# Optimization experiments

Hardware: AMD Instinct MI355X
Metric: run time of the kernel (lower is better)

The kernel has to match this reference:

```python
import jax, jax.numpy as jnp
import numpy as np

BN_EPS = 1e-5
INTERP_EPS = 1e-8


def _bn_relu(x, g, b, m, v):
    # eval-mode BatchNorm1d over channel dim (last axis here) + ReLU
    return jax.nn.relu((x - m) * (g / jnp.sqrt(v + BN_EPS)) + b)


def setup_inputs() -> dict:
    key = jax.random.key(0)
    ks = jax.random.split(key, 12)
    B, N, S, C1, C2 = 4, 16384, 1024, 128, 256
    Cin = C1 + C2  # 384
    H1, H2 = 256, 128
    inp = {
        "xyz1": jax.random.normal(ks[0], (B, N, 3), jnp.float32),
        "xyz2": jax.random.normal(ks[1], (B, S, 3), jnp.float32),
        "points1": jax.random.normal(ks[2], (B, N, C1), jnp.float32),
        "points2": jax.random.normal(ks[3], (B, S, C2), jnp.float32),
        # Conv1d(k=1, bias=False) weights: (out_ch, in_ch)
        "w1": jax.random.normal(ks[4], (H1, Cin), jnp.float32) * (1.0 / np.sqrt(Cin)),
        "g1": jax.random.uniform(ks[5], (H1,), jnp.float32, 0.5, 1.5),
        "b1": jax.random.normal(ks[6], (H1,), jnp.float32) * 0.1,
        "m1": jax.random.normal(ks[7], (H1,), jnp.float32) * 0.1,
        "v1": jax.random.uniform(ks[8], (H1,), jnp.float32, 0.5, 1.5),
        "w2": jax.random.normal(ks[9], (H2, H1), jnp.float32) * (1.0 / np.sqrt(H1)),
        "g2": jax.random.uniform(ks[10], (H2,), jnp.float32, 0.5, 1.5),
        "b2": jax.random.normal(ks[11], (H2,), jnp.float32) * 0.1,
        "m2": jnp.zeros((H2,), jnp.float32),
        "v2": jnp.ones((H2,), jnp.float32),
    }
    return inp


def reference(xyz1, xyz2, points1, points2, w1, g1, b1, m1, v1, w2, g2, b2, m2, v2):
    B, N, _ = xyz1.shape
    S = xyz2.shape[1]
    # squared pairwise distances (B, N, S) via ||a||^2 + ||b||^2 - 2 a.b
    sq = (
        jnp.sum(xyz1 * xyz1, -1)[:, :, None]
        + jnp.sum(xyz2 * xyz2, -1)[:, None, :]
        - 2.0 * jnp.einsum("bnd,bsd->bns", xyz1, xyz2)
    )
    neg_d, idx = jax.lax.top_k(-sq, 3)  # 3 nearest neighbors
    dists = -neg_d  # (B, N, 3) squared distances, ascending
    recip = 1.0 / (dists + INTERP_EPS)
    weight = recip / jnp.sum(recip, -1, keepdims=True)  # (B, N, 3)
    # gather neighbor features: (B, N, 3, C2)
    gathered = points2[jnp.arange(B)[:, None, None], idx]
    interpolated = jnp.einsum("bnk,bnkc->bnc", weight, gathered)
    new_points = jnp.concatenate([points1, interpolated], axis=-1)  # (B, N, Cin)
    h = _bn_relu(jnp.einsum("bnc,dc->bnd", new_points, w1), g1, b1, m1, v1)
    out = _bn_relu(jnp.einsum("bnc,dc->bnd", h, w2), g2, b2, m2, v2)
    return out
```

## Files before the change

### kernel.cpp

```cpp
#include <hip/hip_runtime.h>
#include <math.h>

#define B_    4
#define N_    16384
#define S_    1024
#define C1_   128
#define C2_   256
#define CIN_  384
#define H1_   256
#define H2_   128
#define BN_EPS_     1e-5f
#define INTERP_EPS_ 1e-8f

typedef _Float16 f16;
typedef _Float16 f16x4 __attribute__((ext_vector_type(4)));
typedef _Float16 f16x8 __attribute__((ext_vector_type(8)));
typedef float    f32x4 __attribute__((ext_vector_type(4)));
typedef unsigned int u32;

#define GLD16(g, l) \
  __builtin_amdgcn_global_load_lds((const __attribute__((address_space(1))) void*)(g), \
                                   (__attribute__((address_space(3))) void*)(l), 16, 0, 0)

#define WS_IDXP 0
#define WS_W    262144
#define WS_XI   1048576
#define WS_H    34603008
#define WS_W1F  68157440
#define WS_W2F  68354048
#define WS_SC1  68419584
#define WS_SH1  68420608
#define WS_SC2  68421632
#define WS_SH2  68422144

__global__ __launch_bounds__(256) void prep_kernel(
    const float* __restrict__ w1, const float* __restrict__ w2,
    const float* __restrict__ g1, const float* __restrict__ b1,
    const float* __restrict__ m1, const float* __restrict__ v1,
    const float* __restrict__ g2, const float* __restrict__ b2,
    const float* __restrict__ m2, const float* __restrict__ v2,
    f16* __restrict__ w1f, f16* __restrict__ w2f,
    float* __restrict__ sc1, float* __restrict__ sh1,
    float* __restrict__ sc2, float* __restrict__ sh2)
{
    const int t = blockIdx.x * 256 + threadIdx.x;
    if (t < 98304) {
        w1f[t] = (f16)w1[t];
    } else if (t < 131072) {
        w2f[t - 98304] = (f16)w2[t - 98304];
    } else if (t < 131328) {
        const int c = t - 131072;
        const float s = g1[c] / sqrtf(v1[c] + BN_EPS_);
        sc1[c] = s; sh1[c] = b1[c] - m1[c] * s;
    } else if (t < 131456) {
        const int c = t - 131328;
        const float s = g2[c] / sqrtf(v2[c] + BN_EPS_);
        sc2[c] = s; sh2[c] = b2[c] - m2[c] * s;
    }
}

__device__ __forceinline__ u32 umin_(u32 a, u32 b) { return a < b ? a : b; }
__device__ __forceinline__ u32 umax_(u32 a, u32 b) { return a > b ? a : b; }

#define KINS(k) do { \
    u32 c1 = umax_(s0, (k)); s0 = umin_(s0, (k)); \
    u32 c2 = umax_(s1, c1);  s1 = umin_(s1, c1);  \
    u32 c3 = umax_(s2, c2);  s2 = umin_(s2, c2);  \
    u32 c4 = umax_(s3, c3);  s3 = umin_(s3, c3);  \
    s4 = umin_(s4, c4); } while (0)

#define CSWAP(a_, b_) do { \
    if (rd[b_] < rd[a_] || (rd[b_] == rd[a_] && ri[b_] < ri[a_])) { \
      double td = rd[a_]; rd[a_] = rd[b_]; rd[b_] = td; \
      int ti = ri[a_]; ri[a_] = ri[b_]; ri[b_] = ti; } } while (0)

__global__ __launch_bounds__(256) void topk_kernel(
    const float* __restrict__ xyz1, const float* __restrict__ xyz2,
    u32* __restrict__ idxp_out, float* __restrict__ w_out)
{
    __shared__ float4 q[S_ + 8];
    const int b     = blockIdx.x >> 9;
    const int pbase = (blockIdx.x & 511) << 5;
    const int t     = threadIdx.x;

    for (int i = t; i < S_; i += 256) {
        const float* s = &xyz2[((size_t)b * S_ + i) * 3];
        float4 v; v.x = s[0]; v.y = s[1]; v.z = s[2]; v.w = 0.0f;
        q[i + (i >> 7)] = v;
    }
    __syncthreads();

    const int p     = pbase + (t >> 3);
    const int chunk = t & 7;
    const int qb    = chunk * 129;
    const int ebase = chunk << 7;
    const float* pp = &xyz1[((size_t)b * N_ + p) * 3];
    const float px = pp[0], py = pp[1], pz = pp[2];

    u32 s0 = 0xFFFFFFFFu, s1 = 0xFFFFFFFFu, s2 = 0xFFFFFFFFu,
        s3 = 0xFFFFFFFFu, s4 = 0xFFFFFFFFu;

    for (int i = 0; i < 128; i += 4) {
        #pragma unroll
        for (int u = 0; u < 4; ++u) {
            const float4 c = q[qb + i + u];
            const float dx = px - c.x, dy = py - c.y, dz = pz - c.z;
            const float dd = fmaf(dx, dx, fmaf(dy, dy, dz * dz));
            const u32 k = (__float_as_uint(dd) & 0xFFFFFC00u) | (u32)(ebase + i + u);
            KINS(k);
        }
    }

    #pragma unroll
    for (int msk = 1; msk <= 4; msk <<= 1) {
        u32 e0 = __shfl_xor(s0, msk), e1 = __shfl_xor(s1, msk);
        u32 e2 = __shfl_xor(s2, msk), e3 = __shfl_xor(s3, msk);
        u32 e4 = __shfl_xor(s4, msk);
        KINS(e0); KINS(e1); KINS(e2); KINS(e3); KINS(e4);
    }

    if (chunk == 0) {
        const double px6 = px, py6 = py, pz6 = pz;
        double rd[5]; int ri[5];
        const u32 ks[5] = {s0, s1, s2, s3, s4};
        #pragma unroll
        for (int j = 0; j < 5; ++j) {
            const int si = (int)(ks[j] & 1023u); ri[j] = si;
            const float4 c = q[si + (si >> 7)];
            const double dx = px6 - (double)c.x, dy = py6 - (double)c.y, dz = pz6 - (double)c.z;
            rd[j] = dx * dx + dy * dy + dz * dz;
        }
        CSWAP(0,1); CSWAP(1,2); CSWAP(0,1); CSWAP(2,3); CSWAP(1,2);
        CSWAP(0,1); CSWAP(3,4); CSWAP(2,3); CSWAP(1,2); CSWAP(0,1);
        const float r0 = 1.0f / ((float)rd[0] + INTERP_EPS_);
        const float r1 = 1.0f / ((float)rd[1] + INTERP_EPS_);
        const float r2 = 1.0f / ((float)rd[2] + INTERP_EPS_);
        const float rs = r0 + r1 + r2;
        const int row = b * N_ + p;
        idxp_out[row] = (u32)ri[0] | ((u32)ri[1] << 10) | ((u32)ri[2] << 20);
        w_out[row * 3 + 0] = r0 / rs;
        w_out[row * 3 + 1] = r1 / rs;
        w_out[row * 3 + 2] = r2 / rs;
    }
}

__global__ __launch_bounds__(256) void interp_kernel(
    const float* __restrict__ points2, const u32* __restrict__ idxp,
    const float* __restrict__ wts, f16* __restrict__ xi)
{
    const int row  = blockIdx.x * 8 + (threadIdx.x >> 5);
    const int lane = threadIdx.x & 31;
    const int bb   = row >> 14;
    const u32 u    = idxp[row];
    const int i0 = (int)(u & 1023u), i1 = (int)((u >> 10) & 1023u), i2 = (int)(u >> 20);
    const float w0 = wts[row * 3], w1w = wts[row * 3 + 1], w2w = wts[row * 3 + 2];
    const float* p2b = points2 + (size_t)bb * S_ * C2_;
    const int c0 = lane * 8;

    const float4 a0 = *(const float4*)&p2b[i0 * C2_ + c0];
    const float4 a1 = *(const float4*)&p2b[i0 * C2_ + c0 + 4];
    const float4 b0 = *(const float4*)&p2b[i1 * C2_ + c0];
    const float4 b1 = *(const float4*)&p2b[i1 * C2_ + c0 + 4];
    const float4 d0 = *(const float4*)&p2b[i2 * C2_ + c0];
    const float4 d1 = *(const float4*)&p2b[i2 * C2_ + c0 + 4];

    f16x8 o;
    o[0] = (f16)fmaf(w0, a0.x, fmaf(w1w, b0.x, w2w * d0.x));
    o[1] = (f16)fmaf(w0, a0.y, fmaf(w1w, b0.y, w2w * d0.y));
    o[2] = (f16)fmaf(w0, a0.z, fmaf(w1w, b0.z, w2w * d0.z));
    o[3] = (f16)fmaf(w0, a0.w, fmaf(w1w, b0.w, w2w * d0.w));
    o[4] = (f16)fmaf(w0, a1.x, fmaf(w1w, b1.x, w2w * d1.x));
    o[5] = (f16)fmaf(w0, a1.y, fmaf(w1w, b1.y, w2w * d1.y));
    o[6] = (f16)fmaf(w0, a1.z, fmaf(w1w, b1.z, w2w * d1.z));
    o[7] = (f16)fmaf(w0, a1.w, fmaf(w1w, b1.w, w2w * d1.w));
    *(f16x8*)&xi[(size_t)row * C2_ + c0] = o;
}

__device__ __forceinline__ void mfma_step1(const f16* As, const f16* Bs,
                                           f32x4 (&acc)[4][8],
                                           int wr, int wc, int lrow, int lhi)
{
    f16x8 af[4], bf[8];
    #pragma unroll
    for (int m = 0; m < 4; ++m)
        af[m] = *(const f16x8*)&As[(wr * 64 + m * 16 + lrow) * 32 + lhi * 8];
    #pragma unroll
    for (int n = 0; n < 8; ++n)
        bf[n] = *(const f16x8*)&Bs[(wc * 128 + n * 16 + lrow) * 32 + lhi * 8];
    #pragma unroll
    for (int m = 0; m < 4; ++m)
        #pragma unroll
        for (int n = 0; n < 8; ++n)
            acc[m][n] = __builtin_amdgcn_mfma_f32_16x16x32_f16(af[m], bf[n], acc[m][n], 0, 0, 0);
}

__global__ __launch_bounds__(256, 2) void gemm1_kernel(
    const float* __restrict__ points1, const f16* __restrict__ xi,
    const f16* __restrict__ w1f,
    const float* __restrict__ sc1v, const float* __restrict__ sh1v,
    f16* __restrict__ h)
{
    __shared__ __align__(16) f16 As[2 * 128 * 32];
    __shared__ __align__(16) f16 Bs[2 * 256 * 32];

    const int t = threadIdx.x;
    const int w = t >> 6;
    const int lane = t & 63;
    const int wr = w >> 1, wc = w & 1;
    const int lrow = lane & 15, lhi = lane >> 4;
    const int rowbase = blockIdx.x * 128;

    const int srow = t >> 1, khalf = t & 1;
    const float* p1r = points1 + (size_t)(rowbase + srow) * C1_;

    f32x4 acc[4][8] = {};
    float4 pre0, pre1, pre2, pre3;

    {
        const float* src = p1r + khalf * 16;
        pre0 = *(const float4*)(src + 0);
        pre1 = *(const float4*)(src + 4);
        pre2 = *(const float4*)(src + 8);
        pre3 = *(const float4*)(src + 12);
        f16* asrow = As + srow * 32 + khalf * 16;
        f16x4 o0 = {(f16)pre0.x, (f16)pre0.y, (f16)pre0.z, (f16)pre0.w};
        f16x4 o1 = {(f16)pre1.x, (f16)pre1.y, (f16)pre1.z, (f16)pre1.w};
        f16x4 o2 = {(f16)pre2.x, (f16)pre2.y, (f16)pre2.z, (f16)pre2.w};
        f16x4 o3 = {(f16)pre3.x, (f16)pre3.y, (f16)pre3.z, (f16)pre3.w};
        *(f16x4*)(asrow + 0) = o0; *(f16x4*)(asrow + 4) = o1;
        *(f16x4*)(asrow + 8) = o2; *(f16x4*)(asrow + 12) = o3;
        #pragma unroll
        for (int j = 0; j < 4; ++j) {
            const int c = j * 256 + t;
            GLD16(w1f + (size_t)(c >> 2) * CIN_ + (c & 3) * 8,
                  (char*)Bs + (j * 4096 + w * 1024));
        }
    }
    __syncthreads();

    for (int step = 0; step < 12; ++step) {
        const int pb = step & 1, nb = pb ^ 1;
        const int nkb = (step + 1) * 32;
        const bool has_next = (step < 11);
        const bool nextA = (nkb < C1_);

        if (has_next) {
            if (nextA) {
                const float* src = p1r + nkb + khalf * 16;
                pre0 = *(const float4*)(src + 0);
                pre1 = *(const float4*)(src + 4);
                pre2 = *(const float4*)(src + 8);
                pre3 = *(const float4*)(src + 12);
            } else {
                const int kk = nkb - C1_;
                #pragma unroll
                for (int j = 0; j < 2; ++j) {
                    const int c = j * 256 + t;
                    GLD16(xi + (size_t)(rowbase + (c >> 2)) * C2_ + kk + (c & 3) * 8,
                          (char*)As + (nb * 8192 + j * 4096 + w * 1024));
                }
            }
            #pragma unroll
            for (int j = 0; j < 4; ++j) {
                const int c = j * 256 + t;
                GLD16(w1f + (size_t)(c >> 2) * CIN_ + nkb + (c & 3) * 8,
                      (char*)Bs + (nb * 16384 + j * 4096 + w * 1024));
            }
        }

        mfma_step1(As + pb * 4096, Bs + pb * 8192, acc, wr, wc, lrow, lhi);

        if (has_next && nextA) {
            f16* asrow = As + nb * 4096 + srow * 32 + khalf * 16;
            f16x4 o0 = {(f16)pre0.x, (f16)pre0.y, (f16)pre0.z, (f16)pre0.w};
            f16x4 o1 = {(f16)pre1.x, (f16)pre1.y, (f16)pre1.z, (f16)pre1.w};
            f16x4 o2 = {(f16)pre2.x, (f16)pre2.y, (f16)pre2.z, (f16)pre2.w};
            f16x4 o3 = {(f16)pre3.x, (f16)pre3.y, (f16)pre3.z, (f16)pre3.w};
            *(f16x4*)(asrow + 0) = o0; *(f16x4*)(asrow + 4) = o1;
            *(f16x4*)(asrow + 8) = o2; *(f16x4*)(asrow + 12) = o3;
        }
        __syncthreads();
    }

    #pragma unroll
    for (int n = 0; n < 8; ++n) {
        const int col = wc * 128 + n * 16 + lrow;
        const float sc = sc1v[col], sh = sh1v[col];
        #pragma unroll
        for (int m = 0; m < 4; ++m) {
            const int row0 = rowbase + wr * 64 + m * 16 + lhi * 4;
            #pragma unroll
            for (int i = 0; i < 4; ++i) {
                const float v = fmaxf(fmaf(acc[m][n][i], sc, sh), 0.0f);
                h[(size_t)(row0 + i) * H1_ + col] = (f16)v;
            }
        }
    }
}

__global__ __launch_bounds__(256, 2) void gemm2_kernel(
    const f16* __restrict__ hin, const f16* __restrict__ w2f,
    const float* __restrict__ sc2v, const float* __restrict__ sh2v,
    float* __restrict__ out)
{
    __shared__ __align__(16) f16 As[2 * 128 * 32];
    __shared__ __align__(16) f16 Bs[2 * 128 * 32];

    const int t = threadIdx.x;
    const int w = t >> 6;
    const int lane = t & 63;
    const int wr = w >> 1, wc = w & 1;
    const int lrow = lane & 15, lhi = lane >> 4;
    const int rowbase = blockIdx.x * 128;

    f32x4 acc[4][4] = {};

    #pragma unroll
    for (int j = 0; j < 2; ++j) {
        const int c = j * 256 + t;
        GLD16(hin + (size_t)(rowbase + (c >> 2)) * H1_ + (c & 3) * 8,
              (char*)As + (j * 4096 + w * 1024));
        GLD16(w2f + (size_t)(c >> 2) * H1_ + (c & 3) * 8,
              (char*)Bs + (j * 4096 + w * 1024));
    }
    __syncthreads();

    for (int step = 0; step < 8; ++step) {
        const int pb = step & 1, nb = pb ^ 1;
        const int nkb = (step + 1) * 32;

        if (step < 7) {
            #pragma unroll
            for (int j = 0; j < 2; ++j) {
                const int c = j * 256 + t;
                GLD16(hin + (size_t)(rowbase + (c >> 2)) * H1_ + nkb + (c & 3) * 8,
                      (char*)As + (nb * 8192 + j * 4096 + w * 1024));
                GLD16(w2f + (size_t)(c >> 2) * H1_ + nkb + (c & 3) * 8,
                      (char*)Bs + (nb * 8192 + j * 4096 + w * 1024));
            }
        }

        const f16* Ac = As + pb * 4096;
        const f16* Bc = Bs + pb * 4096;
        f16x8 af[4], bf[4];
        #pragma unroll
        for (int m = 0; m < 4; ++m)
            af[m] = *(const f16x8*)&Ac[(wr * 64 + m * 16 + lrow) * 32 + lhi * 8];
        #pragma unroll
        for (int n = 0; n < 4; ++n)
            bf[n] = *(const f16x8*)&Bc[(wc * 64 + n * 16 + lrow) * 32 + lhi * 8];
        #pragma unroll
        for (int m = 0; m < 4; ++m)
            #pragma unroll
            for (int n = 0; n < 4; ++n)
                acc[m][n] = __builtin_amdgcn_mfma_f32_16x16x32_f16(af[m], bf[n], acc[m][n], 0, 0, 0);

        __syncthreads();
    }

    #pragma unroll
    for (int n = 0; n < 4; ++n) {
        const int col = wc * 64 + n * 16 + lrow;
        const float sc = sc2v[col], sh = sh2v[col];
        #pragma unroll
        for (int m = 0; m < 4; ++m) {
            const int row0 = rowbase + wr * 64 + m * 16 + lhi * 4;
            #pragma unroll
            for (int i = 0; i < 4; ++i) {
                out[(size_t)(row0 + i) * H2_ + col] = fmaxf(fmaf(acc[m][n][i], sc, sh), 0.0f);
            }
        }
    }
}

extern "C" void kernel_launch(void* const* d_in, const int* in_sizes, int n_in,
                              void* d_out, int out_size, void* d_ws, size_t ws_size,
                              hipStream_t stream) {
    const float* xyz1    = (const float*)d_in[0];
    const float* xyz2    = (const float*)d_in[1];
    const float* points1 = (const float*)d_in[2];
    const float* points2 = (const float*)d_in[3];
    const float* w1      = (const float*)d_in[4];
    const float* g1      = (const float*)d_in[5];
    const float* b1      = (const float*)d_in[6];
    const float* m1      = (const float*)d_in[7];
    const float* v1      = (const float*)d_in[8];
    const float* w2      = (const float*)d_in[9];
    const float* g2      = (const float*)d_in[10];
    const float* b2      = (const float*)d_in[11];
    const float* m2      = (const float*)d_in[12];
    const float* v2      = (const float*)d_in[13];
    float* out = (float*)d_out;

    char* ws = (char*)d_ws;
    u32*   idxp_ws = (u32*)(ws + WS_IDXP);
    float* w_ws    = (float*)(ws + WS_W);
    f16*   xi_ws   = (f16*)(ws + WS_XI);
    f16*   h_ws    = (f16*)(ws + WS_H);
    f16*   w1f     = (f16*)(ws + WS_W1F);
    f16*   w2f     = (f16*)(ws + WS_W2F);
    float* sc1     = (float*)(ws + WS_SC1);
    float* sh1     = (float*)(ws + WS_SH1);
    float* sc2     = (float*)(ws + WS_SC2);
    float* sh2     = (float*)(ws + WS_SH2);

    topk_kernel<<<dim3(B_ * (N_ / 32)), dim3(256), 0, stream>>>(xyz1, xyz2, idxp_ws, w_ws);
    prep_kernel<<<dim3(514), dim3(256), 0, stream>>>(w1, w2, g1, b1, m1, v1,
                                                     g2, b2, m2, v2,
                                                     w1f, w2f, sc1, sh1, sc2, sh2);
    interp_kernel<<<dim3(B_ * N_ / 8), dim3(256), 0, stream>>>(points2, idxp_ws, w_ws, xi_ws);
    gemm1_kernel<<<dim3(512), dim3(256), 0, stream>>>(points1, xi_ws, w1f, sc1, sh1, h_ws);
    gemm2_kernel<<<dim3(512), dim3(256), 0, stream>>>(h_ws, w2f, sc2, sh2, out);
}
```

Baseline: 187.6 us.

## Fuse topk+interp+prep into one kernel and gemm1+gemm2 via LDS-resident hidden

Merges the kNN top-k search, weight/BN preparation and feature interpolation into a single front kernel, handing neighbor indices and weights through shared memory instead of global workspace. Fuses the two MLP GEMMs so the hidden activation tile stays in swizzled LDS rather than going through a global f16 buffer. This removes two kernel launches, the idx/weight round trip and the large hidden-activation write and read. In exchange the MLP kernel needs 80KB of dynamic shared memory, which may reduce occupancy. It also relies on the front kernel's prep blocks finishing before mlp_kernel starts, which stream order guarantees.

Result: faster. 183.9 us (-2.0%).

```diff
diff --git a/kernel.cpp b/kernel.cpp
--- a/kernel.cpp
+++ b/kernel.cpp
@@ -22,10 +22,7 @@
   __builtin_amdgcn_global_load_lds((const __attribute__((address_space(1))) void*)(g), \
                                    (__attribute__((address_space(3))) void*)(l), 16, 0, 0)
 
-#define WS_IDXP 0
-#define WS_W    262144
 #define WS_XI   1048576
-#define WS_H    34603008
 #define WS_W1F  68157440
 #define WS_W2F  68354048
 #define WS_SC1  68419584
@@ -33,32 +30,6 @@
 #define WS_SC2  68421632
 #define WS_SH2  68422144
 
-__global__ __launch_bounds__(256) void prep_kernel(
-    const float* __restrict__ w1, const float* __restrict__ w2,
-    const float* __restrict__ g1, const float* __restrict__ b1,
-    const float* __restrict__ m1, const float* __restrict__ v1,
-    const float* __restrict__ g2, const float* __restrict__ b2,
-    const float* __restrict__ m2, const float* __restrict__ v2,
-    f16* __restrict__ w1f, f16* __restrict__ w2f,
-    float* __restrict__ sc1, float* __restrict__ sh1,
-    float* __restrict__ sc2, float* __restrict__ sh2)
-{
-    const int t = blockIdx.x * 256 + threadIdx.x;
-    if (t < 98304) {
-        w1f[t] = (f16)w1[t];
-    } else if (t < 131072) {
-        w2f[t - 98304] = (f16)w2[t - 98304];
-    } else if (t < 131328) {
-        const int c = t - 131072;
-        const float s = g1[c] / sqrtf(v1[c] + BN_EPS_);
-        sc1[c] = s; sh1[c] = b1[c] - m1[c] * s;
-    } else if (t < 131456) {
-        const int c = t - 131328;
-        const float s = g2[c] / sqrtf(v2[c] + BN_EPS_);
-        sc2[c] = s; sh2[c] = b2[c] - m2[c] * s;
-    }
-}
-
 __device__ __forceinline__ u32 umin_(u32 a, u32 b) { return a < b ? a : b; }
 __device__ __forceinline__ u32 umax_(u32 a, u32 b) { return a > b ? a : b; }
 
@@ -74,14 +45,45 @@
       double td = rd[a_]; rd[a_] = rd[b_]; rd[b_] = td; \
       int ti = ri[a_]; ri[a_] = ri[b_]; ri[b_] = ti; } } while (0)
 
-__global__ __launch_bounds__(256) void topk_kernel(
+__global__ __launch_bounds__(256) void front_kernel(
     const float* __restrict__ xyz1, const float* __restrict__ xyz2,
-    u32* __restrict__ idxp_out, float* __restrict__ w_out)
+    const float* __restrict__ points2,
+    const float* __restrict__ w1, const float* __restrict__ w2,
+    const float* __restrict__ g1, const float* __restrict__ b1,
+    const float* __restrict__ m1, const float* __restrict__ v1,
+    const float* __restrict__ g2, const float* __restrict__ b2,
+    const float* __restrict__ m2, const float* __restrict__ v2,
+    f16* __restrict__ xi, f16* __restrict__ w1f, f16* __restrict__ w2f,
+    float* __restrict__ sc1, float* __restrict__ sh1,
+    float* __restrict__ sc2, float* __restrict__ sh2)
 {
+    const int bid = blockIdx.x;
+    const int t   = threadIdx.x;
+
+    if (bid >= 2048) {
+        const int tg = (bid - 2048) * 256 + t;
+        if (tg < 98304) {
+            w1f[tg] = (f16)w1[tg];
+        } else if (tg < 131072) {
+            w2f[tg - 98304] = (f16)w2[tg - 98304];
+        } else if (tg < 131328) {
+            const int c = tg - 131072;
+            const float s = g1[c] / sqrtf(v1[c] + BN_EPS_);
+            sc1[c] = s; sh1[c] = b1[c] - m1[c] * s;
+        } else if (tg < 131456) {
+            const int c = tg - 131328;
+            const float s = g2[c] / sqrtf(v2[c] + BN_EPS_);
+            sc2[c] = s; sh2[c] = b2[c] - m2[c] * s;
+        }
+        return;
+    }
+
     __shared__ float4 q[S_ + 8];
-    const int b     = blockIdx.x >> 9;
-    const int pbase = (blockIdx.x & 511) << 5;
-    const int t     = threadIdx.x;
+    __shared__ int   idr[32][3];
+    __shared__ float wtr[32][3];
+
+    const int b     = bid >> 9;
+    const int pbase = (bid & 511) << 5;
 
     for (int i = t; i < S_; i += 256) {
         const float* s = &xyz2[((size_t)b * S_ + i) * 3];
@@ -90,90 +92,91 @@
     }
     __syncthreads();
 
-    const int p     = pbase + (t >> 3);
-    const int chunk = t & 7;
-    const int qb    = chunk * 129;
-    const int ebase = chunk << 7;
-    const float* pp = &xyz1[((size_t)b * N_ + p) * 3];
-    const float px = pp[0], py = pp[1], pz = pp[2];
-
-    u32 s0 = 0xFFFFFFFFu, s1 = 0xFFFFFFFFu, s2 = 0xFFFFFFFFu,
-        s3 = 0xFFFFFFFFu, s4 = 0xFFFFFFFFu;
-
-    for (int i = 0; i < 128; i += 4) {
-        #pragma unroll
-        for (int u = 0; u < 4; ++u) {
-            const float4 c = q[qb + i + u];
-            const float dx = px - c.x, dy = py - c.y, dz = pz - c.z;
-            const float dd = fmaf(dx, dx, fmaf(dy, dy, dz * dz));
-            const u32 k = (__float_as_uint(dd) & 0xFFFFFC00u) | (u32)(ebase + i + u);
-            KINS(k);
-        }
-    }
-
-    #pragma unroll
-    for (int msk = 1; msk <= 4; msk <<= 1) {
-        u32 e0 = __shfl_xor(s0, msk), e1 = __shfl_xor(s1, msk);
-        u32 e2 = __shfl_xor(s2, msk), e3 = __shfl_xor(s3, msk);
-        u32 e4 = __shfl_xor(s4, msk);
-        KINS(e0); KINS(e1); KINS(e2); KINS(e3); KINS(e4);
-    }
-
-    if (chunk == 0) {
-        const double px6 = px, py6 = py, pz6 = pz;
-        double rd[5]; int ri[5];
-        const u32 ks[5] = {s0, s1, s2, s3, s4};
-        #pragma unroll
-        for (int j = 0; j < 5; ++j) {
-            const int si = (int)(ks[j] & 1023u); ri[j] = si;
-            const float4 c = q[si + (si >> 7)];
-            const double dx = px6 - (double)c.x, dy = py6 - (double)c.y, dz = pz6 - (double)c.z;
-            rd[j] = dx * dx + dy * dy + dz * dz;
-        }
-        CSWAP(0,1); CSWAP(1,2); CSWAP(0,1); CSWAP(2,3); CSWAP(1,2);
-        CSWAP(0,1); CSWAP(3,4); CSWAP(2,3); CSWAP(1,2); CSWAP(0,1);
-        const float r0 = 1.0f / ((float)rd[0] + INTERP_EPS_);
-        const float r1 = 1.0f / ((float)rd[1] + INTERP_EPS_);
-        const float r2 = 1.0f / ((float)rd[2] + INTERP_EPS_);
-        const float rs = r0 + r1 + r2;
-        const int row = b * N_ + p;
-        idxp_out[row] = (u32)ri[0] | ((u32)ri[1] << 10) | ((u32)ri[2] << 20);
-        w_out[row * 3 + 0] = r0 / rs;
-        w_out[row * 3 + 1] = r1 / rs;
-        w_out[row * 3 + 2] = r2 / rs;
-    }
-}
-
-__global__ __launch_bounds__(256) void interp_kernel(
-    const float* __restrict__ points2, const u32* __restrict__ idxp,
-    const float* __restrict__ wts, f16* __restrict__ xi)
-{
-    const int row  = blockIdx.x * 8 + (threadIdx.x >> 5);
-    const int lane = threadIdx.x & 31;
-    const int bb   = row >> 14;
-    const u32 u    = idxp[row];
-    const int i0 = (int)(u & 1023u), i1 = (int)((u >> 10) & 1023u), i2 = (int)(u >> 20);
-    const float w0 = wts[row * 3], w1w = wts[row * 3 + 1], w2w = wts[row * 3 + 2];
-    const float* p2b = points2 + (size_t)bb * S_ * C2_;
-    const int c0 = lane * 8;
-
-    const float4 a0 = *(const float4*)&p2b[i0 * C2_ + c0];
-    const float4 a1 = *(const float4*)&p2b[i0 * C2_ + c0 + 4];
-    const float4 b0 = *(const float4*)&p2b[i1 * C2_ + c0];
-    const float4 b1 = *(const float4*)&p2b[i1 * C2_ + c0 + 4];
-    const float4 d0 = *(const float4*)&p2b[i2 * C2_ + c0];
-    const float4 d1 = *(const float4*)&p2b[i2 * C2_ + c0 + 4];
-
-    f16x8 o;
-    o[0] = (f16)fmaf(w0, a0.x, fmaf(w1w, b0.x, w2w * d0.x));
-    o[1] = (f16)fmaf(w0, a0.y, fmaf(w1w, b0.y, w2w * d0.y));
-    o[2] = (f16)fmaf(w0, a0.z, fmaf(w1w, b0.z, w2w * d0.z));
-    o[3] = (f16)fmaf(w0, a0.w, fmaf(w1w, b0.w, w2w * d0.w));
-    o[4] = (f16)fmaf(w0, a1.x, fmaf(w1w, b1.x, w2w * d1.x));
-    o[5] = (f16)fmaf(w0, a1.y, fmaf(w1w, b1.y, w2w * d1.y));
-    o[6] = (f16)fmaf(w0, a1.z, fmaf(w1w, b1.z, w2w * d1.z));
-    o[7] = (f16)fmaf(w0, a1.w, fmaf(w1w, b1.w, w2w * d1.w));
-    *(f16x8*)&xi[(size_t)row * C2_ + c0] = o;
+    {
+        const int p     = pbase + (t >> 3);
+        const int chunk = t & 7;
+        const int qb    = chunk * 129;
+        const int ebase = chunk << 7;
+        const float* pp = &xyz1[((size_t)b * N_ + p) * 3];
+        const float px = pp[0], py = pp[1], pz = pp[2];
+
+        u32 s0 = 0xFFFFFFFFu, s1 = 0xFFFFFFFFu, s2 = 0xFFFFFFFFu,
+            s3 = 0xFFFFFFFFu, s4 = 0xFFFFFFFFu;
+
+        for (int i = 0; i < 128; i += 4) {
+            #pragma unroll
+            for (int u = 0; u < 4; ++u) {
+                const float4 c = q[qb + i + u];
+                const float dx = px - c.x, dy = py - c.y, dz = pz - c.z;
+                const float dd = fmaf(dx, dx, fmaf(dy, dy, dz * dz));
+                const u32 k = (__float_as_uint(dd) & 0xFFFFFC00u) | (u32)(ebase + i + u);
+                KINS(k);
+            }
+        }
+        #pragma unroll
+        for (int msk = 1; msk <= 4; msk <<= 1) {
+            u32 e0 = __shfl_xor(s0, msk), e1 = __shfl_xor(s1, msk);
+            u32 e2 = __shfl_xor(s2, msk), e3 = __shfl_xor(s3, msk);
+            u32 e4 = __shfl_xor(s4, msk);
+            KINS(e0); KINS(e1); KINS(e2); KINS(e3); KINS(e4);
+        }
+        if (chunk == 0) {
+            const double px6 = px, py6 = py, pz6 = pz;
+            double rd[5]; int ri[5];
+            const u32 ks[5] = {s0, s1, s2, s3, s4};
+            #pragma unroll
+            for (int j = 0; j < 5; ++j) {
+                const int si = (int)(ks[j] & 1023u); ri[j] = si;
+                const float4 c = q[si + (si >> 7)];
+                const double dx = px6 - (double)c.x, dy = py6 - (double)c.y, dz = pz6 - (double)c.z;
+                rd[j] = dx * dx + dy * dy + dz * dz;
+            }
+            CSWAP(0,1); CSWAP(1,2); CSWAP(0,1); CSWAP(2,3); CSWAP(1,2);
+            CSWAP(0,1); CSWAP(3,4); CSWAP(2,3); CSWAP(1,2); CSWAP(0,1);
+            const float r0 = 1.0f / ((float)rd[0] + INTERP_EPS_);
+            const float r1 = 1.0f / ((float)rd[1] + INTERP_EPS_);
+            const float r2 = 1.0f / ((float)rd[2] + INTERP_EPS_);
+            const float rs = r0 + r1 + r2;
+            const int r = t >> 3;
+            idr[r][0] = ri[0]; idr[r][1] = ri[1]; idr[r][2] = ri[2];
+            wtr[r][0] = r0 / rs; wtr[r][1] = r1 / rs; wtr[r][2] = r2 / rs;
+        }
+    }
+    __syncthreads();
+
+    {
+        const int r = t >> 3, j = t & 7;
+        const int i0 = idr[r][0], i1 = idr[r][1], i2 = idr[r][2];
+        const float w0 = wtr[r][0], w1w = wtr[r][1], w2w = wtr[r][2];
+        const float* p2b = points2 + (size_t)b * S_ * C2_;
+        const int c0 = j * 32;
+        float a[32];
+        #pragma unroll
+        for (int g = 0; g < 8; ++g) {
+            const float4 f = *(const float4*)&p2b[i0 * C2_ + c0 + g * 4];
+            a[g*4+0] = w0 * f.x; a[g*4+1] = w0 * f.y; a[g*4+2] = w0 * f.z; a[g*4+3] = w0 * f.w;
+        }
+        #pragma unroll
+        for (int g = 0; g < 8; ++g) {
+            const float4 f = *(const float4*)&p2b[i1 * C2_ + c0 + g * 4];
+            a[g*4+0] = fmaf(w1w, f.x, a[g*4+0]); a[g*4+1] = fmaf(w1w, f.y, a[g*4+1]);
+            a[g*4+2] = fmaf(w1w, f.z, a[g*4+2]); a[g*4+3] = fmaf(w1w, f.w, a[g*4+3]);
+        }
+        #pragma unroll
+        for (int g = 0; g < 8; ++g) {
+            const float4 f = *(const float4*)&p2b[i2 * C2_ + c0 + g * 4];
+            a[g*4+0] = fmaf(w2w, f.x, a[g*4+0]); a[g*4+1] = fmaf(w2w, f.y, a[g*4+1]);
+            a[g*4+2] = fmaf(w2w, f.z, a[g*4+2]); a[g*4+3] = fmaf(w2w, f.w, a[g*4+3]);
+        }
+        const size_t grow = (size_t)(b * N_ + pbase + r);
+        #pragma unroll
+        for (int g8 = 0; g8 < 4; ++g8) {
+            f16x8 o;
+            #pragma unroll
+            for (int e = 0; e < 8; ++e) o[e] = (f16)a[g8 * 8 + e];
+            *(f16x8*)&xi[grow * C2_ + c0 + g8 * 8] = o;
+        }
+    }
 }
 
 __device__ __forceinline__ void mfma_step1(const f16* As, const f16* Bs,
@@ -194,14 +197,17 @@
             acc[m][n] = __builtin_amdgcn_mfma_f32_16x16x32_f16(af[m], bf[n], acc[m][n], 0, 0, 0);
 }
 
-__global__ __launch_bounds__(256, 2) void gemm1_kernel(
+__global__ __launch_bounds__(256, 2) void mlp_kernel(
     const float* __restrict__ points1, const f16* __restrict__ xi,
-    const f16* __restrict__ w1f,
+    const f16* __restrict__ w1f, const f16* __restrict__ w2f,
     const float* __restrict__ sc1v, const float* __restrict__ sh1v,
-    f16* __restrict__ h)
+    const float* __restrict__ sc2v, const float* __restrict__ sh2v,
+    float* __restrict__ out)
 {
-    __shared__ __align__(16) f16 As[2 * 128 * 32];
-    __shared__ __align__(16) f16 Bs[2 * 256 * 32];
+    extern __shared__ __align__(16) char smem[];
+    f16* As = (f16*)smem;
+    f16* Bs = (f16*)(smem + 16384);
+    char* Ht = smem + 16384;
 
     const int t = threadIdx.x;
     const int w = t >> 6;
@@ -283,69 +289,48 @@
     }
 
     #pragma unroll
+    for (int j = 0; j < 2; ++j) {
+        const int c = j * 256 + t;
+        GLD16(w2f + (size_t)(c >> 2) * H1_ + (c & 3) * 8,
+              smem + (j * 4096 + w * 1024));
+    }
+    #pragma unroll
     for (int n = 0; n < 8; ++n) {
         const int col = wc * 128 + n * 16 + lrow;
         const float sc = sc1v[col], sh = sh1v[col];
         #pragma unroll
         for (int m = 0; m < 4; ++m) {
-            const int row0 = rowbase + wr * 64 + m * 16 + lhi * 4;
             #pragma unroll
             for (int i = 0; i < 4; ++i) {
+                const int row = wr * 64 + m * 16 + lhi * 4 + i;
                 const float v = fmaxf(fmaf(acc[m][n][i], sc, sh), 0.0f);
-                h[(size_t)(row0 + i) * H1_ + col] = (f16)v;
-            }
-        }
-    }
-}
-
-__global__ __launch_bounds__(256, 2) void gemm2_kernel(
-    const f16* __restrict__ hin, const f16* __restrict__ w2f,
-    const float* __restrict__ sc2v, const float* __restrict__ sh2v,
-    float* __restrict__ out)
-{
-    __shared__ __align__(16) f16 As[2 * 128 * 32];
-    __shared__ __align__(16) f16 Bs[2 * 128 * 32];
-
-    const int t = threadIdx.x;
-    const int w = t >> 6;
-    const int lane = t & 63;
-    const int wr = w >> 1, wc = w & 1;
-    const int lrow = lane & 15, lhi = lane >> 4;
-    const int rowbase = blockIdx.x * 128;
-
-    f32x4 acc[4][4] = {};
-
-    #pragma unroll
-    for (int j = 0; j < 2; ++j) {
-        const int c = j * 256 + t;
-        GLD16(hin + (size_t)(rowbase + (c >> 2)) * H1_ + (c & 3) * 8,
-              (char*)As + (j * 4096 + w * 1024));
-        GLD16(w2f + (size_t)(c >> 2) * H1_ + (c & 3) * 8,
-              (char*)Bs + (j * 4096 + w * 1024));
+                const u32 byteoff = (u32)(row * 512 + col * 2) ^ ((u32)(row & 7) << 4);
+                *(f16*)(Ht + byteoff) = (f16)v;
+            }
+        }
     }
     __syncthreads();
 
+    f32x4 acc2[4][4] = {};
     for (int step = 0; step < 8; ++step) {
         const int pb = step & 1, nb = pb ^ 1;
         const int nkb = (step + 1) * 32;
-
         if (step < 7) {
             #pragma unroll
             for (int j = 0; j < 2; ++j) {
                 const int c = j * 256 + t;
-                GLD16(hin + (size_t)(rowbase + (c >> 2)) * H1_ + nkb + (c & 3) * 8,
-                      (char*)As + (nb * 8192 + j * 4096 + w * 1024));
                 GLD16(w2f + (size_t)(c >> 2) * H1_ + nkb + (c & 3) * 8,
-                      (char*)Bs + (nb * 8192 + j * 4096 + w * 1024));
-            }
-        }
-
-        const f16* Ac = As + pb * 4096;
-        const f16* Bc = Bs + pb * 4096;
+                      smem + (nb * 8192 + j * 4096 + w * 1024));
+            }
+        }
         f16x8 af[4], bf[4];
         #pragma unroll
-        for (int m = 0; m < 4; ++m)
-            af[m] = *(const f16x8*)&Ac[(wr * 64 + m * 16 + lrow) * 32 + lhi * 8];
+        for (int m = 0; m < 4; ++m) {
+            const int row = wr * 64 + m * 16 + lrow;
+            const u32 byteoff = (u32)(row * 512 + (step * 32 + lhi * 8) * 2) ^ ((u32)(row & 7) << 4);
+            af[m] = *(const f16x8*)(Ht + byteoff);
+        }
+        const f16* Bc = (const f16*)(smem + pb * 8192);
         #pragma unroll
         for (int n = 0; n < 4; ++n)
             bf[n] = *(const f16x8*)&Bc[(wc * 64 + n * 16 + lrow) * 32 + lhi * 8];
@@ -353,8 +338,7 @@
         for (int m = 0; m < 4; ++m)
             #pragma unroll
             for (int n = 0; n < 4; ++n)
-                acc[m][n] = __builtin_amdgcn_mfma_f32_16x16x32_f16(af[m], bf[n], acc[m][n], 0, 0, 0);
-
+                acc2[m][n] = __builtin_amdgcn_mfma_f32_16x16x32_f16(af[m], bf[n], acc2[m][n], 0, 0, 0);
         __syncthreads();
     }
 
@@ -367,7 +351,7 @@
             const int row0 = rowbase + wr * 64 + m * 16 + lhi * 4;
             #pragma unroll
             for (int i = 0; i < 4; ++i) {
-                out[(size_t)(row0 + i) * H2_ + col] = fmaxf(fmaf(acc[m][n][i], sc, sh), 0.0f);
+                out[(size_t)(row0 + i) * H2_ + col] = fmaxf(fmaf(acc2[m][n][i], sc, sh), 0.0f);
             }
         }
     }
@@ -393,22 +377,17 @@
     float* out = (float*)d_out;
 
     char* ws = (char*)d_ws;
-    u32*   idxp_ws = (u32*)(ws + WS_IDXP);
-    float* w_ws    = (float*)(ws + WS_W);
-    f16*   xi_ws   = (f16*)(ws + WS_XI);
-    f16*   h_ws    = (f16*)(ws + WS_H);
-    f16*   w1f     = (f16*)(ws + WS_W1F);
-    f16*   w2f     = (f16*)(ws + WS_W2F);
-    float* sc1     = (float*)(ws + WS_SC1);
-    float* sh1     = (float*)(ws + WS_SH1);
-    float* sc2     = (float*)(ws + WS_SC2);
-    float* sh2     = (float*)(ws + WS_SH2);
-
-    topk_kernel<<<dim3(B_ * (N_ / 32)), dim3(256), 0, stream>>>(xyz1, xyz2, idxp_ws, w_ws);
-    prep_kernel<<<dim3(514), dim3(256), 0, stream>>>(w1, w2, g1, b1, m1, v1,
-                                                     g2, b2, m2, v2,
-                                                     w1f, w2f, sc1, sh1, sc2, sh2);
-    interp_kernel<<<dim3(B_ * N_ / 8), dim3(256), 0, stream>>>(points2, idxp_ws, w_ws, xi_ws);
-    gemm1_kernel<<<dim3(512), dim3(256), 0, stream>>>(points1, xi_ws, w1f, sc1, sh1, h_ws);
-    gemm2_kernel<<<dim3(512), dim3(256), 0, stream>>>(h_ws, w2f, sc2, sh2, out);
+    f16*   xi_ws = (f16*)(ws + WS_XI);
+    f16*   w1f   = (f16*)(ws + WS_W1F);
+    f16*   w2f   = (f16*)(ws + WS_W2F);
+    float* sc1   = (float*)(ws + WS_SC1);
+    float* sh1   = (float*)(ws + WS_SH1);
+    float* sc2   = (float*)(ws + WS_SC2);
+    float* sh2   = (float*)(ws + WS_SH2);
+
+    front_kernel<<<dim3(2562), dim3(256), 0, stream>>>(
+        xyz1, xyz2, points2, w1, w2, g1, b1, m1, v1, g2, b2, m2, v2,
+        xi_ws, w1f, w2f, sc1, sh1, sc2, sh2);
+    mlp_kernel<<<dim3(512), dim3(256), 81920, stream>>>(
+        points1, xi_ws, w1f, w2f, sc1, sh1, sc2, sh2, out);
 }
```
